# Performance work log

Hardware: AMD Instinct MI355X
Metric: run time of the kernel (lower is better)

Reference implementation:

```python
import jax, jax.numpy as jnp
import numpy as np

N, P, C = 100000, 64, 128
DIST_TH = 0.1


def setup_inputs() -> dict:
    key = jax.random.key(0)
    ks = jax.random.split(key, 12)
    xyz = jax.random.uniform(ks[0], (N, 3), jnp.float32) * 10.0  # room coords in [0,10)^3
    feature = jax.random.normal(ks[1], (N, C), jnp.float32)
    center = jax.random.uniform(ks[2], (P, 3), jnp.float32) * 10.0
    normal = jax.random.normal(ks[3], (P, 3), jnp.float32)
    normal = normal / jnp.linalg.norm(normal, axis=1, keepdims=True)
    pmin = center - 1.5  # axis-aligned extent used on axes 0,1
    pmax = center + 1.5
    inp = {
        'feature': feature, 'xyz': xyz,
        'plane_center': center, 'plane_normal': normal,
        'plane_min': pmin, 'plane_max': pmax,
        'W1': jax.random.normal(ks[4], (C, 2 * C), jnp.float32) * (1.0 / np.sqrt(C)),
        's1': jnp.ones((2 * C,), jnp.float32), 'b1': jnp.zeros((2 * C,), jnp.float32),
        'W2': jax.random.normal(ks[5], (2 * C, C), jnp.float32) * (1.0 / np.sqrt(2 * C)),
        's2': jnp.ones((C,), jnp.float32), 'b2': jnp.zeros((C,), jnp.float32),
        'W3': jax.random.normal(ks[6], (C, 1), jnp.float32) * (1.0 / np.sqrt(C)),
        'b3': jnp.zeros((1,), jnp.float32),
        'Wa': jax.random.normal(ks[7], (C, C), jnp.float32) * (1.0 / np.sqrt(C)),
        'Wm': jax.random.normal(ks[8], (C, C), jnp.float32) * (1.0 / np.sqrt(C)),
        'bm': jnp.zeros((C,), jnp.float32),
    }
    return inp


def reference(feature, xyz, plane_center, plane_normal, plane_min, plane_max,
              W1, s1, b1, W2, s2, b2, W3, b3, Wa, Wm, bm):
    # pointwise MLP (shared across planes): fc1 (conv+BN+ReLU), fc2 (conv+BN+ReLU)
    h = jax.nn.relu((feature @ W1) * s1 + b1)          # [N, 2C]
    h2 = jax.nn.relu((h @ W2) * s2 + b2)               # [N, C] == plane_feature
    logit = (h2 @ W3 + b3)[:, 0]                        # [N] fc3 logits (plane_result)

    # per-plane point membership masks (dense [N, P])
    proj = xyz @ plane_normal.T                         # [N, P]
    offs = jnp.sum(plane_center * plane_normal, axis=1) # [P]
    dist_mask = jnp.abs(proj - offs[None, :]) < DIST_TH
    rng = ((xyz[:, None, 0] >= plane_min[None, :, 0]) & (xyz[:, None, 0] < plane_max[None, :, 0]) &
           (xyz[:, None, 1] >= plane_min[None, :, 1]) & (xyz[:, None, 1] < plane_max[None, :, 1]))
    mask = dist_mask & rng                              # [N, P]

    on_sel = jax.nn.sigmoid(logit) > 0.5                # [N]
    on_mask = (mask & on_sel[:, None]).astype(feature.dtype)
    off_mask = (mask & ~on_sel[:, None]).astype(feature.dtype)

    # attention pooling: masked softmax over points, per plane, per channel
    a = h2 @ Wa                                         # [N, C] att activations
    e = jnp.exp(a - jnp.max(a, axis=0, keepdims=True))  # stable exp, [N, C]
    eh = e * h2

    def att_pool(m):                                    # m: [N, P] float
        num = jnp.einsum('np,nc->pc', m, eh)
        den = jnp.einsum('np,nc->pc', m, e)
        agg = num / (den + 1e-9)                        # masked-softmax weighted sum
        return jax.nn.relu(agg @ Wm + bm)               # att_pooling.mlp (conv+ReLU)

    ori = jnp.concatenate([plane_center, plane_normal, plane_min, plane_max], axis=1)  # [P, 12]
    on_feat = jnp.concatenate([att_pool(on_mask), ori], axis=1)    # [P, C+12]
    off_feat = jnp.concatenate([att_pool(off_mask), ori], axis=1)  # [P, C+12]
    return logit, on_feat, off_feat
```

## Files before the change

### kernel.cpp

```cpp
#include <hip/hip_runtime.h>

#define NPTS 100000
#define P 64
#define C 128
#define NBLK 1563
#define BLK_REC 48
#define LIST_CAP 4096
#define CNT_STRIDE 16

typedef __bf16 bf16_t;
typedef __bf16 bf16x8 __attribute__((ext_vector_type(8)));
typedef float floatx4 __attribute__((ext_vector_type(4)));


__global__ __launch_bounds__(256) void prep_kernel(
    const float* __restrict__ W1, const float* __restrict__ s1,
    const float* __restrict__ W2, const float* __restrict__ s2,
    const float* __restrict__ Wa,
    bf16_t* __restrict__ W1t, bf16_t* __restrict__ W2t, bf16_t* __restrict__ Wat,
    unsigned* __restrict__ cnt)
{
  int i0 = blockIdx.x * blockDim.x + threadIdx.x;
  int stride = gridDim.x * blockDim.x;
  for (int i = i0; i < 256 * 128; i += stride) {
    int n = i >> 7, k = i & 127;
    W1t[i] = (bf16_t)(W1[k * 256 + n] * s1[n]);
  }
  for (int i = i0; i < 128 * 256; i += stride) {
    int n = i >> 8, k = i & 255;
    W2t[i] = (bf16_t)(W2[k * 128 + n] * s2[n]);
  }
  for (int i = i0; i < 128 * 128; i += stride) {
    int n = i >> 7, k = i & 127;
    Wat[i] = (bf16_t)(Wa[k * 128 + n]);
  }
  if (i0 < 64 * CNT_STRIDE) cnt[i0] = 0;
}

__global__ __launch_bounds__(256, 4) void main_kernel(
    const float* __restrict__ feature, const float* __restrict__ xyz,
    const float* __restrict__ b1, const float* __restrict__ b2,
    const float* __restrict__ W3, const float* __restrict__ b3,
    const float* __restrict__ ctr, const float* __restrict__ nrm,
    const float* __restrict__ pmn, const float* __restrict__ pmx,
    const bf16_t* __restrict__ W1t, const bf16_t* __restrict__ W2t,
    const bf16_t* __restrict__ Wat,
    unsigned* __restrict__ cnt, unsigned* __restrict__ list,
    bf16_t* __restrict__ rec, float* __restrict__ out_logit)
{
  __shared__ __align__(16) char smem[36368];
  bf16_t* A1   = (bf16_t*)smem;
  bf16_t* Hh   = (bf16_t*)(smem + 17408);
  bf16_t* aB   = (bf16_t*)(smem + 17408);
  float*  w3S  = (float*)(smem + 34816);
  float*  xyzS = (float*)(smem + 35328);
  float*  lgS  = (float*)(smem + 36096);
  unsigned* blkCnt = (unsigned*)(smem + 36352);

  const int tid  = threadIdx.x;
  const int wave = tid >> 6, lane = tid & 63;
  const int quad = lane >> 4, l16 = lane & 15;
  const int m0 = blockIdx.x * 64;

  if (tid < 128) w3S[tid] = W3[tid];
  if (tid < 192) {
    int gi = m0 * 3 + tid;
    xyzS[tid] = (gi < NPTS * 3) ? xyz[gi] : 0.f;
  }
  if (tid == 0) *blkCnt = 0;

  for (int i = tid; i < 64 * 32; i += 256) {
    int r = i >> 5, c4 = i & 31;
    float4 v = make_float4(0.f, 0.f, 0.f, 0.f);
    if (m0 + r < NPTS) v = *(const float4*)(feature + (size_t)(m0 + r) * C + c4 * 4);
    bf16_t* dst = A1 + r * 136 + c4 * 4;
    dst[0] = (bf16_t)v.x; dst[1] = (bf16_t)v.y; dst[2] = (bf16_t)v.z; dst[3] = (bf16_t)v.w;
  }
  __syncthreads();

  const floatx4 zero4 = {0.f, 0.f, 0.f, 0.f};

  floatx4 acc2[4][2];
#pragma unroll
  for (int mt = 0; mt < 4; ++mt) { acc2[mt][0] = zero4; acc2[mt][1] = zero4; }

#pragma unroll
  for (int half = 0; half < 2; ++half) {
    floatx4 acc1[4][2];
#pragma unroll
    for (int mt = 0; mt < 4; ++mt) { acc1[mt][0] = zero4; acc1[mt][1] = zero4; }
#pragma unroll
    for (int kt = 0; kt < 4; ++kt) {
      bf16x8 af[4], bfr[2];
#pragma unroll
      for (int mt = 0; mt < 4; ++mt)
        af[mt] = *(const bf16x8*)(A1 + (mt * 16 + l16) * 136 + kt * 32 + quad * 8);
#pragma unroll
      for (int nt = 0; nt < 2; ++nt)
        bfr[nt] = *(const bf16x8*)(W1t + (size_t)(half * 128 + wave * 32 + nt * 16 + l16) * 128 + kt * 32 + quad * 8);
#pragma unroll
      for (int mt = 0; mt < 4; ++mt)
#pragma unroll
        for (int nt = 0; nt < 2; ++nt)
          acc1[mt][nt] = __builtin_amdgcn_mfma_f32_16x16x32_bf16(af[mt], bfr[nt], acc1[mt][nt], 0, 0, 0);
    }
#pragma unroll
    for (int nt = 0; nt < 2; ++nt) {
      int hcol = wave * 32 + nt * 16 + l16;
      float bias = b1[half * 128 + hcol];
#pragma unroll
      for (int mt = 0; mt < 4; ++mt)
#pragma unroll
        for (int r = 0; r < 4; ++r) {
          float hv = fmaxf(acc1[mt][nt][r] + bias, 0.f);
          Hh[(mt * 16 + quad * 4 + r) * 136 + hcol] = (bf16_t)hv;
        }
    }
    __syncthreads();

#pragma unroll
    for (int kt = 0; kt < 4; ++kt) {
      bf16x8 af[4], bfr[2];
#pragma unroll
      for (int mt = 0; mt < 4; ++mt)
        af[mt] = *(const bf16x8*)(Hh + (mt * 16 + l16) * 136 + kt * 32 + quad * 8);
#pragma unroll
      for (int nt = 0; nt < 2; ++nt)
        bfr[nt] = *(const bf16x8*)(W2t + (size_t)(wave * 32 + nt * 16 + l16) * 256 + half * 128 + kt * 32 + quad * 8);
#pragma unroll
      for (int mt = 0; mt < 4; ++mt)
#pragma unroll
        for (int nt = 0; nt < 2; ++nt)
          acc2[mt][nt] = __builtin_amdgcn_mfma_f32_16x16x32_bf16(af[mt], bfr[nt], acc2[mt][nt], 0, 0, 0);
    }
    if (half == 0)
      __syncthreads();
  }

#pragma unroll
  for (int nt = 0; nt < 2; ++nt) {
    int col = wave * 32 + nt * 16 + l16;
    float bias = b2[col];
#pragma unroll
    for (int mt = 0; mt < 4; ++mt)
#pragma unroll
      for (int r = 0; r < 4; ++r) {
        float hv = fmaxf(acc2[mt][nt][r] + bias, 0.f);
        A1[(mt * 16 + quad * 4 + r) * 136 + col] = (bf16_t)hv;
      }
  }
  __syncthreads();

  {
    const int m = tid >> 2, g = tid & 3, c0g = g * 32;
    const int mg = m0 + m;
    float lsum = 0.f;
#pragma unroll 8
    for (int c = 0; c < 32; ++c)
      lsum += (float)A1[m * 136 + c0g + c] * w3S[c0g + c];
    lsum += __shfl_xor(lsum, 1);
    lsum += __shfl_xor(lsum, 2);
    if (g == 0) {
      float lg = lsum + b3[0];
      lgS[m] = lg;
      if (mg < NPTS) out_logit[mg] = lg;
    }
  }

  {
    floatx4 acca[4][2];
#pragma unroll
    for (int mt = 0; mt < 4; ++mt) { acca[mt][0] = zero4; acca[mt][1] = zero4; }
#pragma unroll
    for (int kt = 0; kt < 4; ++kt) {
      bf16x8 af[4], bfr[2];
#pragma unroll
      for (int mt = 0; mt < 4; ++mt)
        af[mt] = *(const bf16x8*)(A1 + (mt * 16 + l16) * 136 + kt * 32 + quad * 8);
#pragma unroll
      for (int nt = 0; nt < 2; ++nt)
        bfr[nt] = *(const bf16x8*)(Wat + (size_t)(wave * 32 + nt * 16 + l16) * 128 + kt * 32 + quad * 8);
#pragma unroll
      for (int mt = 0; mt < 4; ++mt)
#pragma unroll
        for (int nt = 0; nt < 2; ++nt)
          acca[mt][nt] = __builtin_amdgcn_mfma_f32_16x16x32_bf16(af[mt], bfr[nt], acca[mt][nt], 0, 0, 0);
    }
#pragma unroll
    for (int nt = 0; nt < 2; ++nt) {
      int col = wave * 32 + nt * 16 + l16;
#pragma unroll
      for (int mt = 0; mt < 4; ++mt)
#pragma unroll
        for (int r = 0; r < 4; ++r)
          aB[(mt * 16 + quad * 4 + r) * 136 + col] = (bf16_t)acca[mt][nt][r];
    }
  }
  __syncthreads();

  {
    const float nx = nrm[lane * 3], ny = nrm[lane * 3 + 1], nz = nrm[lane * 3 + 2];
    const float offsP = ctr[lane * 3] * nx + ctr[lane * 3 + 1] * ny + ctr[lane * 3 + 2] * nz;
    const float mnx = pmn[lane * 3], mny = pmn[lane * 3 + 1];
    const float mxx = pmx[lane * 3], mxy = pmx[lane * 3 + 1];

    for (int s = 0; s < 16; ++s) {
      const int pt = wave * 16 + s;
      const bool valid = (m0 + pt) < NPTS;
      const float x = xyzS[pt * 3], y = xyzS[pt * 3 + 1], z = xyzS[pt * 3 + 2];
      const float proj = x * nx + y * ny + z * nz;
      const bool hit = valid && (fabsf(proj - offsP) < 0.1f) &&
                       (x >= mnx) && (x < mxx) && (y >= mny) && (y < mxy);
      unsigned long long mball = __ballot(hit);
      if (!mball) continue;

      unsigned slot = 0;
      if (lane == 0) slot = atomicAdd(blkCnt, 1u);
      slot = (unsigned)__shfl((int)slot, 0);
      if (slot >= BLK_REC) continue;

      const unsigned ridx = (unsigned)blockIdx.x * BLK_REC + slot;
      const int sel = (lgS[pt] > 0.f) ? 0 : 1;
      const unsigned ap = ((const unsigned*)(aB + pt * 136))[lane];
      const unsigned hp = ((const unsigned*)(A1 + pt * 136))[lane];
      unsigned* dst = (unsigned*)(rec + (size_t)ridx * 256);
      dst[lane]      = ap;
      dst[64 + lane] = hp;
      if (hit) {
        unsigned idx = atomicAdd(&cnt[lane * CNT_STRIDE], 1u);
        if (idx < LIST_CAP)
          list[lane * LIST_CAP + idx] = (ridx << 1) | (unsigned)sel;
      }
    }
  }
}

__global__ __launch_bounds__(256) void pool2_kernel(
    const unsigned* __restrict__ cnt, const unsigned* __restrict__ list,
    const bf16_t* __restrict__ rec, float* __restrict__ partial)
{
  const int plane = blockIdx.x >> 4;
  const int chunk = blockIdx.x & 15;
  const int tid = threadIdx.x, wave = tid >> 6, lane = tid & 63;

  __shared__ float accS[4][128];
  for (int i = tid; i < 512; i += 256) ((float*)accS)[i] = 0.f;
  __syncthreads();

  unsigned n = cnt[plane * CNT_STRIDE];
  if (n > LIST_CAP) n = LIST_CAP;
  const unsigned* lp = list + plane * LIST_CAP;

  float nOn0 = 0, nOn1 = 0, dOn0 = 0, dOn1 = 0;
  float nOf0 = 0, nOf1 = 0, dOf0 = 0, dOf1 = 0;

  for (unsigned e = (unsigned)(chunk * 4 + wave); e < n; e += 64) {
    const unsigned ent = lp[e];
    const unsigned row = ent >> 1;
    const unsigned* r32 = (const unsigned*)(rec + (size_t)row * 256);
    const unsigned ap = r32[lane];
    const unsigned hp = r32[64 + lane];
    const float a0 = __uint_as_float(ap << 16);
    const float a1 = __uint_as_float(ap & 0xffff0000u);
    const float h0 = __uint_as_float(hp << 16);
    const float h1 = __uint_as_float(hp & 0xffff0000u);
    const float e0 = __expf(a0), e1 = __expf(a1);
    if (!(ent & 1)) { nOn0 += e0 * h0; nOn1 += e1 * h1; dOn0 += e0; dOn1 += e1; }
    else            { nOf0 += e0 * h0; nOf1 += e1 * h1; dOf0 += e0; dOf1 += e1; }
  }

  atomicAdd(&accS[0][lane * 2],     nOn0);
  atomicAdd(&accS[0][lane * 2 + 1], nOn1);
  atomicAdd(&accS[1][lane * 2],     dOn0);
  atomicAdd(&accS[1][lane * 2 + 1], dOn1);
  atomicAdd(&accS[2][lane * 2],     nOf0);
  atomicAdd(&accS[2][lane * 2 + 1], nOf1);
  atomicAdd(&accS[3][lane * 2],     dOf0);
  atomicAdd(&accS[3][lane * 2 + 1], dOf1);
  __syncthreads();

  float* dst = partial + (size_t)blockIdx.x * 512;
  for (int i = tid; i < 512; i += 256) dst[i] = ((float*)accS)[i];
}

__global__ __launch_bounds__(128) void finalize_kernel(
    const float* __restrict__ partial,
    const float* __restrict__ Wm, const float* __restrict__ bm,
    const float* __restrict__ ctr, const float* __restrict__ nrm,
    const float* __restrict__ pmn, const float* __restrict__ pmx,
    float* __restrict__ out)
{
  int sel = blockIdx.x >> 6, p = blockIdx.x & 63;
  int j = threadIdx.x;
  float num = 0.f, den = 0.f;
  const float* bp = partial + (size_t)p * 16 * 512 + sel * 2 * 128;
#pragma unroll
  for (int k = 0; k < 16; ++k) {
    num += bp[k * 512 + j];
    den += bp[k * 512 + 128 + j];
  }
  __shared__ float aggS[128];
  aggS[j] = num / (den + 1e-9f);
  __syncthreads();
  float s = bm[j];
#pragma unroll 4
  for (int c = 0; c < C; ++c) s += aggS[c] * Wm[c * C + j];
  s = fmaxf(s, 0.f);
  float* dst = out + NPTS + sel * (P * 140) + p * 140;
  dst[j] = s;
  if (j < 12) {
    float v;
    if (j < 3)      v = ctr[p * 3 + j];
    else if (j < 6) v = nrm[p * 3 + j - 3];
    else if (j < 9) v = pmn[p * 3 + j - 6];
    else            v = pmx[p * 3 + j - 9];
    dst[C + j] = v;
  }
}

extern "C" void kernel_launch(void* const* d_in, const int* in_sizes, int n_in,
                              void* d_out, int out_size, void* d_ws, size_t ws_size,
                              hipStream_t stream)
{
  const float* feature = (const float*)d_in[0];
  const float* xyz     = (const float*)d_in[1];
  const float* ctr     = (const float*)d_in[2];
  const float* nrm     = (const float*)d_in[3];
  const float* pmn     = (const float*)d_in[4];
  const float* pmx     = (const float*)d_in[5];
  const float* W1      = (const float*)d_in[6];
  const float* s1      = (const float*)d_in[7];
  const float* b1      = (const float*)d_in[8];
  const float* W2      = (const float*)d_in[9];
  const float* s2      = (const float*)d_in[10];
  const float* b2      = (const float*)d_in[11];
  const float* W3      = (const float*)d_in[12];
  const float* b3      = (const float*)d_in[13];
  const float* Wa      = (const float*)d_in[14];
  const float* Wm      = (const float*)d_in[15];
  const float* bm      = (const float*)d_in[16];
  float* out = (float*)d_out;

  char* ws = (char*)d_ws;
  bf16_t*   W1t  = (bf16_t*)(ws);
  bf16_t*   W2t  = (bf16_t*)(ws + 65536);
  bf16_t*   Wat  = (bf16_t*)(ws + 131072);
  unsigned* cnt  = (unsigned*)(ws + 163840);
  unsigned* list = (unsigned*)(ws + 167936);
  bf16_t*   rec  = (bf16_t*)(ws + 1216512);
  float* partial = (float*)(ws + 1216512 + (size_t)NBLK * BLK_REC * 512);

  prep_kernel<<<64, 256, 0, stream>>>(W1, s1, W2, s2, Wa, W1t, W2t, Wat, cnt);
  main_kernel<<<NBLK, 256, 0, stream>>>(
      feature, xyz, b1, b2, W3, b3, ctr, nrm, pmn, pmx,
      W1t, W2t, Wat, cnt, list, rec, out);
  pool2_kernel<<<64 * 16, 256, 0, stream>>>(cnt, list, rec, partial);
  finalize_kernel<<<128, 128, 0, stream>>>(partial, Wm, bm, ctr, nrm, pmn, pmx, out);
}
```

Measured before the change: 189.1 us.

## Replace global per-plane atomic lists with per-block slot lists and compaction

Removes global atomic counters for plane membership lists; each wave writes hits into fixed per-block, per-plane slots initialized with sentinels. The pooling kernel scans its block range, compacts valid entries into shared memory via shared atomics, then accumulates. This trades global atomic contention for a large sentinel fill in the prep kernel and a larger list scan in pooling.

```diff
diff --git a/kernel.cpp b/kernel.cpp
--- a/kernel.cpp
+++ b/kernel.cpp
@@ -5,8 +5,9 @@
 #define C 128
 #define NBLK 1563
 #define BLK_REC 48
-#define LIST_CAP 4096
-#define CNT_STRIDE 16
+#define LIST_SLOTS 32
+#define WAVE_SLOTS 8
+#define CHK 98
 
 typedef __bf16 bf16_t;
 typedef __bf16 bf16x8 __attribute__((ext_vector_type(8)));
@@ -18,7 +19,7 @@
     const float* __restrict__ W2, const float* __restrict__ s2,
     const float* __restrict__ Wa,
     bf16_t* __restrict__ W1t, bf16_t* __restrict__ W2t, bf16_t* __restrict__ Wat,
-    unsigned* __restrict__ cnt)
+    unsigned* __restrict__ list)
 {
   int i0 = blockIdx.x * blockDim.x + threadIdx.x;
   int stride = gridDim.x * blockDim.x;
@@ -34,7 +35,9 @@
     int n = i >> 7, k = i & 127;
     Wat[i] = (bf16_t)(Wa[k * 128 + n]);
   }
-  if (i0 < 64 * CNT_STRIDE) cnt[i0] = 0;
+  uint4* l4 = (uint4*)list;
+  const uint4 sent = make_uint4(0xFFFFFFFFu, 0xFFFFFFFFu, 0xFFFFFFFFu, 0xFFFFFFFFu);
+  for (int i = i0; i < 64 * NBLK * LIST_SLOTS / 4; i += stride) l4[i] = sent;
 }
 
 __global__ __launch_bounds__(256, 4) void main_kernel(
@@ -45,8 +48,8 @@
     const float* __restrict__ pmn, const float* __restrict__ pmx,
     const bf16_t* __restrict__ W1t, const bf16_t* __restrict__ W2t,
     const bf16_t* __restrict__ Wat,
-    unsigned* __restrict__ cnt, unsigned* __restrict__ list,
-    bf16_t* __restrict__ rec, float* __restrict__ out_logit)
+    unsigned* __restrict__ list, bf16_t* __restrict__ rec,
+    float* __restrict__ out_logit)
 {
   __shared__ __align__(16) char smem[36368];
   bf16_t* A1   = (bf16_t*)smem;
@@ -203,6 +206,10 @@
     const float offsP = ctr[lane * 3] * nx + ctr[lane * 3 + 1] * ny + ctr[lane * 3 + 2] * nz;
     const float mnx = pmn[lane * 3], mny = pmn[lane * 3 + 1];
     const float mxx = pmx[lane * 3], mxy = pmx[lane * 3 + 1];
+    unsigned* myList = list + (size_t)lane * (NBLK * LIST_SLOTS)
+                            + (unsigned)blockIdx.x * LIST_SLOTS
+                            + wave * WAVE_SLOTS;
+    int lcnt = 0;
 
     for (int s = 0; s < 16; ++s) {
       const int pt = wave * 16 + s;
@@ -226,36 +233,49 @@
       unsigned* dst = (unsigned*)(rec + (size_t)ridx * 256);
       dst[lane]      = ap;
       dst[64 + lane] = hp;
-      if (hit) {
-        unsigned idx = atomicAdd(&cnt[lane * CNT_STRIDE], 1u);
-        if (idx < LIST_CAP)
-          list[lane * LIST_CAP + idx] = (ridx << 1) | (unsigned)sel;
+      if (hit && lcnt < WAVE_SLOTS) {
+        myList[lcnt] = (ridx << 1) | (unsigned)sel;
+        ++lcnt;
       }
     }
   }
 }
 
 __global__ __launch_bounds__(256) void pool2_kernel(
-    const unsigned* __restrict__ cnt, const unsigned* __restrict__ list,
-    const bf16_t* __restrict__ rec, float* __restrict__ partial)
+    const unsigned* __restrict__ list, const bf16_t* __restrict__ rec,
+    float* __restrict__ partial)
 {
   const int plane = blockIdx.x >> 4;
   const int chunk = blockIdx.x & 15;
   const int tid = threadIdx.x, wave = tid >> 6, lane = tid & 63;
 
   __shared__ float accS[4][128];
+  __shared__ unsigned compS[CHK * LIST_SLOTS];
+  __shared__ unsigned cntS;
   for (int i = tid; i < 512; i += 256) ((float*)accS)[i] = 0.f;
-  __syncthreads();
-
-  unsigned n = cnt[plane * CNT_STRIDE];
-  if (n > LIST_CAP) n = LIST_CAP;
-  const unsigned* lp = list + plane * LIST_CAP;
+  if (tid == 0) cntS = 0;
+  __syncthreads();
+
+  const int t0 = chunk * CHK;
+  const int t1 = (t0 + CHK < NBLK) ? t0 + CHK : NBLK;
+  const int nent = (t1 - t0) * LIST_SLOTS;
+  const unsigned* lp = list + (size_t)plane * (NBLK * LIST_SLOTS) + t0 * LIST_SLOTS;
+
+  for (int e = tid; e < nent; e += 256) {
+    unsigned v = lp[e];
+    if (v != 0xFFFFFFFFu) {
+      unsigned pos = atomicAdd(&cntS, 1u);
+      compS[pos] = v;
+    }
+  }
+  __syncthreads();
+  const unsigned n = cntS;
 
   float nOn0 = 0, nOn1 = 0, dOn0 = 0, dOn1 = 0;
   float nOf0 = 0, nOf1 = 0, dOf0 = 0, dOf1 = 0;
 
-  for (unsigned e = (unsigned)(chunk * 4 + wave); e < n; e += 64) {
-    const unsigned ent = lp[e];
+  for (unsigned e = (unsigned)wave; e < n; e += 4) {
+    const unsigned ent = compS[e];
     const unsigned row = ent >> 1;
     const unsigned* r32 = (const unsigned*)(rec + (size_t)row * 256);
     const unsigned ap = r32[lane];
@@ -345,15 +365,14 @@
   bf16_t*   W1t  = (bf16_t*)(ws);
   bf16_t*   W2t  = (bf16_t*)(ws + 65536);
   bf16_t*   Wat  = (bf16_t*)(ws + 131072);
-  unsigned* cnt  = (unsigned*)(ws + 163840);
-  unsigned* list = (unsigned*)(ws + 167936);
-  bf16_t*   rec  = (bf16_t*)(ws + 1216512);
-  float* partial = (float*)(ws + 1216512 + (size_t)NBLK * BLK_REC * 512);
-
-  prep_kernel<<<64, 256, 0, stream>>>(W1, s1, W2, s2, Wa, W1t, W2t, Wat, cnt);
+  unsigned* list = (unsigned*)(ws + 163840);
+  bf16_t*   rec  = (bf16_t*)(ws + 12967936);
+  float* partial = (float*)(ws + 12967936 + (size_t)NBLK * BLK_REC * 512);
+
+  prep_kernel<<<64, 256, 0, stream>>>(W1, s1, W2, s2, Wa, W1t, W2t, Wat, list);
   main_kernel<<<NBLK, 256, 0, stream>>>(
       feature, xyz, b1, b2, W3, b3, ctr, nrm, pmn, pmx,
-      W1t, W2t, Wat, cnt, list, rec, out);
-  pool2_kernel<<<64 * 16, 256, 0, stream>>>(cnt, list, rec, partial);
+      W1t, W2t, Wat, list, rec, out);
+  pool2_kernel<<<64 * 16, 256, 0, stream>>>(list, rec, partial);
   finalize_kernel<<<128, 128, 0, stream>>>(partial, Wm, bm, ctr, nrm, pmn, pmx, out);
 }
```

Result: slower. 193.0 us (+2.0%).
